# Kernel tuning notes

Measured on AMD Instinct MI355X. Metric: run time of the kernel, lower is better.

## Reference

```python
import jax, jax.numpy as jnp
import numpy as np

B, T, D, R, WP, WF, NS = 32, 256, 512, 4, 8, 8, 2
N = B * T


def _build_graph():
    # Windowed dialog graph: edge j -> i for j in [i-WP, i+WF], j != i.
    # rel = (0 if same speaker else 2) + (1 if j > i else 0)
    rng = np.random.RandomState(0)
    spk = rng.randint(0, NS, size=(B, T))
    src, dst, rel = [], [], []
    for b in range(B):
        off = b * T
        for i in range(T):
            for j in range(max(0, i - WP), min(T - 1, i + WF) + 1):
                if j == i:
                    continue
                r = (0 if spk[b, j] == spk[b, i] else 2) + int(j > i)
                src.append(off + j)
                dst.append(off + i)
                rel.append(r)
    return np.array([src, dst], dtype=np.int32), np.array(rel, dtype=np.int32)


def setup_inputs() -> dict:
    key = jax.random.key(0)
    ks = jax.random.split(key, 16)
    ei, et = _build_graph()
    s = 0.02
    f32 = jnp.float32
    return {
        "x": jax.random.normal(ks[0], (B, T, D), f32),
        "edge_index": jnp.asarray(ei),
        "edge_type": jnp.asarray(et),
        # RGCNConv params (aggr='mean', root_weight=True, bias=True)
        "W_rel": jax.random.normal(ks[1], (R, D, D), f32) * s,
        "W_root": jax.random.normal(ks[2], (D, D), f32) * s,
        "b_rgcn": jnp.zeros((D,), f32),
        # TransformerConv params (heads=1, concat=True, root_weight=True)
        "Wq": jax.random.normal(ks[3], (D, D), f32) * s,
        "bq": jnp.zeros((D,), f32),
        "Wk": jax.random.normal(ks[4], (D, D), f32) * s,
        "bk": jnp.zeros((D,), f32),
        "Wv": jax.random.normal(ks[5], (D, D), f32) * s,
        "bv": jnp.zeros((D,), f32),
        "Wskip": jax.random.normal(ks[6], (D, D), f32) * s,
        "bskip": jnp.zeros((D,), f32),
        # LayerNorm params
        "gamma": jnp.ones((D,), f32),
        "beta": jnp.zeros((D,), f32),
    }


def _gnn(x, edge_index, edge_type, W_rel, W_root, b_rgcn,
         Wq, bq, Wk, bk, Wv, bv, Wskip, bskip, gamma, beta):
    nodes = x.reshape(N, D)  # all dia_len == T, so valid nodes = all nodes
    src, dst = edge_index[0], edge_index[1]

    # --- RGCNConv: per-relation linear + mean aggregation over each relation ---
    xW = jnp.einsum("nd,rde->nre", nodes, W_rel)          # [N, R, D]
    msg = xW[src, edge_type]                                # [E, D]
    comb = dst * R + edge_type                              # group (dst, rel)
    cnt = jax.ops.segment_sum(jnp.ones(src.shape, nodes.dtype), comb,
                              num_segments=N * R).reshape(N, R)
    inv = 1.0 / jnp.maximum(cnt, 1.0)
    msg = msg * inv[dst, edge_type][:, None]
    ho = jax.ops.segment_sum(msg, dst, num_segments=N) + nodes @ W_root + b_rgcn

    # --- TransformerConv (heads=1): edge attention + scatter-softmax ---
    q = ho @ Wq + bq
    k = ho @ Wk + bk
    v = ho @ Wv + bv
    logits = jnp.sum(q[dst] * k[src], axis=-1) / jnp.sqrt(jnp.asarray(D, ho.dtype))
    mx = jax.ops.segment_max(logits, dst, num_segments=N)
    mx = jnp.where(jnp.isfinite(mx), mx, 0.0)               # nodes w/o in-edges
    ex = jnp.exp(logits - mx[dst])
    den = jax.ops.segment_sum(ex, dst, num_segments=N)
    alpha = ex / jnp.maximum(den[dst], 1e-16)
    agg = jax.ops.segment_sum(alpha[:, None] * v[src], dst, num_segments=N)
    h = agg + ho @ Wskip + bskip

    h = jax.nn.leaky_relu(h, 0.01)                          # dropout = identity (eval)
    out = x + h.reshape(B, T, D)
    mu = out.mean(-1, keepdims=True)
    var = out.var(-1, keepdims=True)
    return (out - mu) / jnp.sqrt(var + 1e-5) * gamma + beta


def reference(x, edge_index, edge_type, W_rel, W_root, b_rgcn,
              Wq, bq, Wk, bk, Wv, bv, Wskip, bskip, gamma, beta):
    out = _gnn(x, edge_index, edge_type, W_rel, W_root, b_rgcn,
               Wq, bq, Wk, bk, Wv, bv, Wskip, bskip, gamma, beta)
    return out, jnp.asarray(0.0, x.dtype)  # graph_cl_loss == 0 in eval path
```

## Files before the change

kernel.cpp:

```cpp
#include <hip/hip_runtime.h>

typedef unsigned short u16;
typedef __attribute__((ext_vector_type(8))) short s16x8;
typedef __attribute__((ext_vector_type(4))) float f32x4;

__device__ __forceinline__ float bf2f(u16 u) {
  union { unsigned int i; float f; } v; v.i = ((unsigned int)u) << 16; return v.f;
}
__device__ __forceinline__ u16 f2bf(float f) {
  union { float f; unsigned int i; } v; v.f = f;
  unsigned int r = (v.i + 0x7FFFu + ((v.i >> 16) & 1u)) >> 16;
  return (u16)r;
}
__device__ __forceinline__ void async16(const void* g, void* l) {
  __builtin_amdgcn_global_load_lds((const __attribute__((address_space(1))) void*)g,
                                   (__attribute__((address_space(3))) void*)l, 16, 0, 0);
}

__global__ __launch_bounds__(256) void prep_kernel(
    const float* __restrict__ W_rel, const float* __restrict__ W_root,
    const float* __restrict__ Wq, const float* __restrict__ Wk,
    const float* __restrict__ Wv, const float* __restrict__ Wskip,
    const float* __restrict__ bq, const float* __restrict__ bk,
    const float* __restrict__ bv, const float* __restrict__ bskip,
    const float* __restrict__ x,
    u16* __restrict__ Bt1, u16* __restrict__ Bt2, float* __restrict__ bias2,
    u16* __restrict__ Acat, int Nn,
    const int* __restrict__ dst, int E, int* __restrict__ rs, int* __restrict__ re)
{
  const int b = (int)blockIdx.x;
  const int tid = threadIdx.x;
  if (b < 576) {
    __shared__ float tile[64][65];
    const float* S;
    u16* D;
    int ldD;
    long dbase;
    if (b < 320) {
      const int kt = b >> 3, et = b & 7;
      const int r0 = kt * 64, c0 = et * 64;
      S = (r0 < 2048) ? (W_rel + (long)r0 * 512 + c0)
                      : (W_root + (long)(r0 - 2048) * 512 + c0);
      D = Bt1; ldD = 2560; dbase = (long)c0 * 2560 + r0;
    } else {
      const int b2 = b - 320;
      const int jt = b2 >> 3, kt = b2 & 7;
      const int j0 = jt * 64, k0 = kt * 64;
      const int which = j0 >> 9, col0 = j0 & 511;
      const float* W = (which == 0) ? Wq : (which == 1) ? Wk : (which == 2) ? Wv : Wskip;
      S = W + (long)k0 * 512 + col0;
      D = Bt2; ldD = 512; dbase = (long)j0 * 512 + k0;
    }
    const int lc = tid & 63;
#pragma unroll
    for (int i = 0; i < 16; ++i) {
      const int r = (tid >> 6) * 16 + i;
      tile[r][lc] = S[(long)r * 512 + lc];
    }
    __syncthreads();
    const int oc2 = (tid & 31) * 2;
#pragma unroll
    for (int i = 0; i < 8; ++i) {
      const int orow = (tid >> 5) + i * 8;
      const unsigned int pk = (unsigned int)f2bf(tile[oc2][orow]) |
                              ((unsigned int)f2bf(tile[oc2 + 1][orow]) << 16);
      *(unsigned int*)(D + dbase + (long)orow * ldD + oc2) = pk;
    }
  } else if (b == 576) {
#pragma unroll
    for (int i = 0; i < 8; ++i) {
      const int j = tid + i * 256;
      const int which = j >> 9, col = j & 511;
      const float* bb = (which == 0) ? bq : (which == 1) ? bk : (which == 2) ? bv : bskip;
      bias2[j] = bb[col];
    }
  } else if (b < 4673) {
    const long u = ((long)(b - 577) * 256 + tid) * 4;
    if (u < (long)Nn * 512) {
      const float4 v = *(const float4*)(x + u);
      const unsigned int p0 = (unsigned int)f2bf(v.x) | ((unsigned int)f2bf(v.y) << 16);
      const unsigned int p1 = (unsigned int)f2bf(v.z) | ((unsigned int)f2bf(v.w) << 16);
      unsigned int* dp = (unsigned int*)(Acat + ((long)(u >> 9)) * 2560 + 2048 + (u & 511));
      dp[0] = p0; dp[1] = p1;
    }
  } else {
    const int e = (b - 4673) * 256 + tid;
    if (e < E) {
      const int d = dst[e];
      if (e == 0 || dst[e - 1] != d) rs[d] = e;
      if (e == E - 1 || dst[e + 1] != d) re[d] = e + 1;
    }
  }
}

__global__ __launch_bounds__(256) void aggregate_kernel(
    const u16* __restrict__ Acat_ro, const int* __restrict__ src,
    const int* __restrict__ etype, const int* __restrict__ rs,
    const int* __restrict__ re, u16* __restrict__ Acat)
{
  __shared__ int s_src[16];
  __shared__ int s_rel[16];
  const int q = (int)gridDim.x >> 3;
  const int bid = (int)blockIdx.x;
  const int i = (bid & 7) * q + (bid >> 3);
  const int tid = threadIdx.x;
  const int s = rs[i];
  int nE = re[i] - s;
  if (nE > 16) nE = 16;
  if (tid < nE) { s_src[tid] = src[s + tid]; s_rel[tid] = etype[s + tid]; }
  __syncthreads();

  float2 acc[4] = {};
  int cnt[4] = {0, 0, 0, 0};
  for (int t = 0; t < nE; ++t) {
    const int sj = s_src[t];
    const int rel = s_rel[t];
    const unsigned int pk = *(const unsigned int*)(Acat_ro + (long)sj * 2560 + 2048 + tid * 2);
    const float vx = bf2f((u16)pk), vy = bf2f((u16)(pk >> 16));
#pragma unroll
    for (int r = 0; r < 4; ++r)
      if (rel == r) { acc[r].x += vx; acc[r].y += vy; cnt[r]++; }
  }

  const long base = (long)i * 2560 + tid * 2;
#pragma unroll
  for (int r = 0; r < 4; ++r) {
    const float inv = 1.0f / fmaxf((float)cnt[r], 1.0f);
    const unsigned int pk = ((unsigned int)f2bf(acc[r].y * inv) << 16) | f2bf(acc[r].x * inv);
    *(unsigned int*)(Acat + base + r * 512) = pk;
  }
}

__global__ __launch_bounds__(512, 4) void gemm_bt_kernel(
    const u16* __restrict__ A, const u16* __restrict__ Bt,
    const float* __restrict__ bias, u16* __restrict__ C,
    const int M, const int N, const int K)
{
  __shared__ u16 lds[2][2][128 * 64];
  const int tid = threadIdx.x;
  const int lane = tid & 63, wid = tid >> 6;
  const int nbn = N >> 7;
  const int q = (int)gridDim.x >> 3;
  const int bid = (int)blockIdx.x;
  const int swz = (bid & 7) * q + (bid >> 3);
  const int bm = swz / nbn, bn = swz % nbn;
  const int wr = wid >> 2, wc = wid & 3;

  f32x4 acc[4][2] = {};

  const int srow = tid >> 3;
  const int sch = tid & 7;
  const long a_row0 = (long)bm * 128;
  const long b_row0 = (long)bn * 128;
  const int lds_wbase = wid * 512;

  auto STAGE = [&](int buf, int kt) {
#pragma unroll
    for (int it = 0; it < 2; ++it) {
      const int row = it * 64 + srow;
      const int lch = sch ^ (row & 7);
      async16(A  + (a_row0 + row) * K + kt + lch * 8, &lds[buf][0][it * 4096 + lds_wbase]);
      async16(Bt + (b_row0 + row) * K + kt + lch * 8, &lds[buf][1][it * 4096 + lds_wbase]);
    }
  };

  const int nt = K >> 6;
  STAGE(0, 0);
  int cur = 0;
  for (int t = 0; t < nt; ++t) {
    asm volatile("s_waitcnt vmcnt(0)" ::: "memory");
    __builtin_amdgcn_s_barrier();
    if (t + 1 < nt) STAGE(cur ^ 1, (t + 1) << 6);
#pragma unroll
    for (int kk = 0; kk < 2; ++kk) {
      s16x8 af[4], bfr[2];
#pragma unroll
      for (int mi = 0; mi < 4; ++mi) {
        const int row = wr * 64 + mi * 16 + (lane & 15);
        const int cb = (kk * 64 + ((lane >> 4) << 4)) ^ ((row & 7) << 4);
        af[mi] = *(const s16x8*)((const char*)&lds[cur][0][0] + row * 128 + cb);
      }
#pragma unroll
      for (int ni = 0; ni < 2; ++ni) {
        const int row = wc * 32 + ni * 16 + (lane & 15);
        const int cb = (kk * 64 + ((lane >> 4) << 4)) ^ ((row & 7) << 4);
        bfr[ni] = *(const s16x8*)((const char*)&lds[cur][1][0] + row * 128 + cb);
      }
      __builtin_amdgcn_s_setprio(1);
#pragma unroll
      for (int mi = 0; mi < 4; ++mi)
#pragma unroll
        for (int ni = 0; ni < 2; ++ni)
          acc[mi][ni] = __builtin_amdgcn_mfma_f32_16x16x32_bf16(af[mi], bfr[ni], acc[mi][ni], 0, 0, 0);
      __builtin_amdgcn_s_setprio(0);
    }
    cur ^= 1;
  }

#pragma unroll
  for (int mi = 0; mi < 4; ++mi) {
    const int row0 = bm * 128 + wr * 64 + mi * 16 + ((lane >> 4) << 2);
#pragma unroll
    for (int ni = 0; ni < 2; ++ni) {
      const int col = bn * 128 + wc * 32 + ni * 16 + (lane & 15);
      const float bv = bias[col];
#pragma unroll
      for (int j = 0; j < 4; ++j)
        C[(long)(row0 + j) * N + col] = f2bf(acc[mi][ni][j] + bv);
    }
  }
}

__global__ __launch_bounds__(512, 2) void gemm256_kernel(
    const u16* __restrict__ A, const u16* __restrict__ Bt,
    const float* __restrict__ bias, u16* __restrict__ C,
    const int M, const int N, const int K)
{
  __shared__ u16 lds[2][2][256 * 64];
  const int tid = threadIdx.x;
  const int lane = tid & 63, wid = tid >> 6;
  const int nbn = N >> 8;
  const int q = (int)gridDim.x >> 3;
  const int bid = (int)blockIdx.x;
  const int swz = (bid & 7) * q + (bid >> 3);
  const int bm = swz / nbn, bn = swz % nbn;
  const int wr = wid >> 2, wc = wid & 3;

  f32x4 acc[8][4] = {};

  const int srow = tid >> 3;
  const int sch = tid & 7;
  const long a_row0 = (long)bm * 256;
  const long b_row0 = (long)bn * 256;
  const int lds_wbase = wid * 512;

  auto STAGE = [&](int buf, int kt) {
#pragma unroll
    for (int it = 0; it < 4; ++it) {
      const int row = it * 64 + srow;
      const int lch = sch ^ (srow & 7);
      async16(A  + (a_row0 + row) * K + kt + lch * 8, &lds[buf][0][it * 4096 + lds_wbase]);
      async16(Bt + (b_row0 + row) * K + kt + lch * 8, &lds[buf][1][it * 4096 + lds_wbase]);
    }
  };

  const int nt = K >> 6;
  STAGE(0, 0);
  int cur = 0;
  for (int t = 0; t < nt; ++t) {
    asm volatile("s_waitcnt vmcnt(0)" ::: "memory");
    __builtin_amdgcn_s_barrier();
    s16x8 bfr[4][2];
#pragma unroll
    for (int p = 0; p < 4; ++p) {
      s16x8 af[2][2];
#pragma unroll
      for (int i2 = 0; i2 < 2; ++i2) {
        const int row = wr * 128 + (p * 2 + i2) * 16 + (lane & 15);
#pragma unroll
        for (int kk = 0; kk < 2; ++kk) {
          const int cb = (kk * 64 + ((lane >> 4) << 4)) ^ ((row & 7) << 4);
          af[i2][kk] = *(const s16x8*)((const char*)&lds[cur][0][0] + row * 128 + cb);
        }
      }
      if (p == 0) {
#pragma unroll
        for (int ni = 0; ni < 4; ++ni) {
          const int row = wc * 64 + ni * 16 + (lane & 15);
#pragma unroll
          for (int kk = 0; kk < 2; ++kk) {
            const int cb = (kk * 64 + ((lane >> 4) << 4)) ^ ((row & 7) << 4);
            bfr[ni][kk] = *(const s16x8*)((const char*)&lds[cur][1][0] + row * 128 + cb);
          }
        }
        if (t + 1 < nt) STAGE(cur ^ 1, (t + 1) << 6);
      }
      __builtin_amdgcn_s_barrier();
      asm volatile("s_waitcnt lgkmcnt(0)" ::: "memory");
      __builtin_amdgcn_sched_barrier(0);
      __builtin_amdgcn_s_setprio(1);
#pragma unroll
      for (int i2 = 0; i2 < 2; ++i2)
#pragma unroll
        for (int ni = 0; ni < 4; ++ni)
#pragma unroll
          for (int kk = 0; kk < 2; ++kk)
            acc[p * 2 + i2][ni] = __builtin_amdgcn_mfma_f32_16x16x32_bf16(
                af[i2][kk], bfr[ni][kk], acc[p * 2 + i2][ni], 0, 0, 0);
      __builtin_amdgcn_s_setprio(0);
      __builtin_amdgcn_s_barrier();
    }
    cur ^= 1;
  }

#pragma unroll
  for (int mi = 0; mi < 8; ++mi) {
    const int row0 = bm * 256 + wr * 128 + mi * 16 + ((lane >> 4) << 2);
#pragma unroll
    for (int ni = 0; ni < 4; ++ni) {
      const int col = bn * 256 + wc * 64 + ni * 16 + (lane & 15);
      const float bv = bias[col];
#pragma unroll
      for (int j = 0; j < 4; ++j)
        C[(long)(row0 + j) * N + col] = f2bf(acc[mi][ni][j] + bv);
    }
  }
}

__global__ __launch_bounds__(256) void attn_wave_kernel(
    const u16* __restrict__ qkvs, const int* __restrict__ src,
    const int* __restrict__ rs, const int* __restrict__ re,
    const float* __restrict__ x, const float* __restrict__ gamma,
    const float* __restrict__ beta, float* __restrict__ out,
    float* __restrict__ scl)
{
  __shared__ float sm[4][16];
  __shared__ int s_src[4][16];
  const int bid = (int)blockIdx.x;
  const int tid = threadIdx.x;
  const int lane = tid & 63, wid = tid >> 6;
  const int q = (int)gridDim.x >> 3;
  const int blk = (bid & 7) * q + (bid >> 3);
  const int i = blk * 4 + wid;
  if (bid == 0 && tid == 0) scl[0] = 0.0f;

  const int s0 = rs[i];
  int ne = re[i] - s0;
  if (ne > 16) ne = 16;
  const int g16 = lane & 15;
  const int eg  = lane >> 4;
  if (lane < ne) s_src[wid][lane] = src[s0 + lane];

  float qv[32];
#pragma unroll
  for (int c = 0; c < 4; ++c) {
    const s16x8 q8 = *(const s16x8*)(qkvs + (long)i * 2048 + c * 128 + g16 * 8);
#pragma unroll
    for (int u = 0; u < 8; ++u) qv[c * 8 + u] = bf2f((u16)q8[u]);
  }

#pragma unroll
  for (int round = 0; round < 4; ++round) {
    const int e = round * 4 + eg;
    float dp = 0.f;
    if (e < ne) {
      const long rb = (long)s_src[wid][e] * 2048 + 512;
#pragma unroll
      for (int c = 0; c < 4; ++c) {
        const s16x8 k8 = *(const s16x8*)(qkvs + rb + c * 128 + g16 * 8);
#pragma unroll
        for (int u = 0; u < 8; ++u) dp += qv[c * 8 + u] * bf2f((u16)k8[u]);
      }
    }
#pragma unroll
    for (int m = 1; m <= 8; m <<= 1) dp += __shfl_xor(dp, m);
    if (g16 == 0 && e < ne) sm[wid][e] = dp * 0.04419417382415922f;
  }
  {
    const float v = (lane < ne) ? sm[wid][lane] : -1e30f;
    float mx = v;
#pragma unroll
    for (int m = 1; m <= 8; m <<= 1) mx = fmaxf(mx, __shfl_xor(mx, m, 16));
    const float ex = (lane < ne) ? expf(v - mx) : 0.f;
    float den = ex;
#pragma unroll
    for (int m = 1; m <= 8; m <<= 1) den += __shfl_xor(den, m, 16);
    if (lane < ne) sm[wid][lane] = ex / fmaxf(den, 1e-16f);
  }

  const int d8 = lane * 8;
  float a[8] = {};
  for (int e = 0; e < ne; ++e) {
    const float al = sm[wid][e];
    const s16x8 v8 = *(const s16x8*)(qkvs + (long)s_src[wid][e] * 2048 + 1024 + d8);
#pragma unroll
    for (int u = 0; u < 8; ++u) a[u] += al * bf2f((u16)v8[u]);
  }
  const s16x8 sk8 = *(const s16x8*)(qkvs + (long)i * 2048 + 1536 + d8);
  const float4 x0 = *(const float4*)(x + (long)i * 512 + d8);
  const float4 x1 = *(const float4*)(x + (long)i * 512 + d8 + 4);
  float o[8];
  float s = 0.f, s2 = 0.f;
#pragma unroll
  for (int u = 0; u < 8; ++u) {
    float h = a[u] + bf2f((u16)sk8[u]);
    h = (h > 0.f) ? h : 0.01f * h;
    const float xx = (u < 4) ? ((const float*)&x0)[u] : ((const float*)&x1)[u - 4];
    o[u] = xx + h;
    s += o[u];
    s2 += o[u] * o[u];
  }
#pragma unroll
  for (int m = 32; m >= 1; m >>= 1) { s += __shfl_xor(s, m); s2 += __shfl_xor(s2, m); }
  const float mean = s * (1.f / 512.f);
  const float var = s2 * (1.f / 512.f) - mean * mean;
  const float rstd = rsqrtf(var + 1e-5f);
  const float4 g0 = *(const float4*)(gamma + d8), g1 = *(const float4*)(gamma + d8 + 4);
  const float4 b0 = *(const float4*)(beta + d8),  b1 = *(const float4*)(beta + d8 + 4);
  float4 r0, r1;
  r0.x = (o[0] - mean) * rstd * g0.x + b0.x;
  r0.y = (o[1] - mean) * rstd * g0.y + b0.y;
  r0.z = (o[2] - mean) * rstd * g0.z + b0.z;
  r0.w = (o[3] - mean) * rstd * g0.w + b0.w;
  r1.x = (o[4] - mean) * rstd * g1.x + b1.x;
  r1.y = (o[5] - mean) * rstd * g1.y + b1.y;
  r1.z = (o[6] - mean) * rstd * g1.z + b1.z;
  r1.w = (o[7] - mean) * rstd * g1.w + b1.w;
  *(float4*)(out + (long)i * 512 + d8) = r0;
  *(float4*)(out + (long)i * 512 + d8 + 4) = r1;
}

extern "C" void kernel_launch(void* const* d_in, const int* in_sizes, int n_in,
                              void* d_out, int out_size, void* d_ws, size_t ws_size,
                              hipStream_t stream) {
  const float* x      = (const float*)d_in[0];
  const int*   ei     = (const int*)d_in[1];
  const int*   et     = (const int*)d_in[2];
  const float* W_rel  = (const float*)d_in[3];
  const float* W_root = (const float*)d_in[4];
  const float* b_rgcn = (const float*)d_in[5];
  const float* Wq     = (const float*)d_in[6];
  const float* bq     = (const float*)d_in[7];
  const float* Wk     = (const float*)d_in[8];
  const float* bk     = (const float*)d_in[9];
  const float* Wv     = (const float*)d_in[10];
  const float* bv     = (const float*)d_in[11];
  const float* Wskip  = (const float*)d_in[12];
  const float* bskip  = (const float*)d_in[13];
  const float* gamma  = (const float*)d_in[14];
  const float* beta   = (const float*)d_in[15];
  const int E  = in_sizes[2];
  const int Nn = in_sizes[0] / 512;
  const int* srcA = ei;
  const int* dstA = ei + E;

  char* p = (char*)d_ws;
  u16* Acat   = (u16*)p;   p += (size_t)Nn * 2560 * 2;
  u16* Bt1    = (u16*)p;   p += (size_t)512 * 2560 * 2;
  u16* Bt2    = (u16*)p;   p += (size_t)2048 * 512 * 2;
  float* bias2= (float*)p; p += (size_t)2048 * 4;
  u16* ho     = (u16*)p;   p += (size_t)Nn * 512 * 2;
  u16* qkvs   = (u16*)p;   p += (size_t)Nn * 2048 * 2;
  int* rs     = (int*)p;   p += (size_t)Nn * 4;
  int* re     = (int*)p;   p += (size_t)Nn * 4;

  const int FB = (E + 255) / 256;
  const int prep_blocks = 4673 + FB;

  prep_kernel<<<prep_blocks, 256, 0, stream>>>(W_rel, W_root, Wq, Wk, Wv, Wskip,
                                               bq, bk, bv, bskip, x, Bt1, Bt2, bias2, Acat, Nn,
                                               dstA, E, rs, re);
  aggregate_kernel<<<Nn, 256, 0, stream>>>(Acat, srcA, et, rs, re, Acat);
  gemm_bt_kernel<<<(Nn / 128) * (512 >> 7), 512, 0, stream>>>(Acat, Bt1, b_rgcn, ho, Nn, 512, 2560);
  gemm256_kernel<<<(Nn / 256) * (2048 >> 8), 512, 0, stream>>>(ho, Bt2, bias2, qkvs, Nn, 2048, 512);
  attn_wave_kernel<<<Nn / 4, 256, 0, stream>>>(qkvs, srcA, rs, re, x, gamma, beta,
                                               (float*)d_out, (float*)d_out + (size_t)Nn * 512);
}
```

Baseline: 114.8 us.

## Double K-tile depth in GEMM and restructure LDS read/MFMA phases with barriers

```diff
diff --git a/kernel.cpp b/kernel.cpp
--- a/kernel.cpp
+++ b/kernel.cpp
@@ -131,12 +131,12 @@
   }
 }
 
-__global__ __launch_bounds__(512, 4) void gemm_bt_kernel(
+__global__ __launch_bounds__(512, 2) void gemm_bt_kernel(
     const u16* __restrict__ A, const u16* __restrict__ Bt,
     const float* __restrict__ bias, u16* __restrict__ C,
     const int M, const int N, const int K)
 {
-  __shared__ u16 lds[2][2][128 * 64];
+  __shared__ u16 lds[2][2][128 * 128];
   const int tid = threadIdx.x;
   const int lane = tid & 63, wid = tid >> 6;
   const int nbn = N >> 7;
@@ -148,51 +148,66 @@
 
   f32x4 acc[4][2] = {};
 
-  const int srow = tid >> 3;
-  const int sch = tid & 7;
   const long a_row0 = (long)bm * 128;
   const long b_row0 = (long)bn * 128;
-  const int lds_wbase = wid * 512;
 
   auto STAGE = [&](int buf, int kt) {
 #pragma unroll
-    for (int it = 0; it < 2; ++it) {
-      const int row = it * 64 + srow;
-      const int lch = sch ^ (row & 7);
-      async16(A  + (a_row0 + row) * K + kt + lch * 8, &lds[buf][0][it * 4096 + lds_wbase]);
-      async16(Bt + (b_row0 + row) * K + kt + lch * 8, &lds[buf][1][it * 4096 + lds_wbase]);
+    for (int it = 0; it < 4; ++it) {
+      const int rbase = it * 32 + wid * 4;
+      const int row = rbase + (lane >> 4);
+      const int lch = (lane & 15) ^ (row & 7);
+      async16(A  + (a_row0 + row) * K + kt + lch * 8, &lds[buf][0][rbase * 128]);
+      async16(Bt + (b_row0 + row) * K + kt + lch * 8, &lds[buf][1][rbase * 128]);
     }
   };
 
-  const int nt = K >> 6;
+  const int nt = K >> 7;
   STAGE(0, 0);
   int cur = 0;
   for (int t = 0; t < nt; ++t) {
     asm volatile("s_waitcnt vmcnt(0)" ::: "memory");
     __builtin_amdgcn_s_barrier();
-    if (t + 1 < nt) STAGE(cur ^ 1, (t + 1) << 6);
-#pragma unroll
-    for (int kk = 0; kk < 2; ++kk) {
-      s16x8 af[4], bfr[2];
+    s16x8 bfr[2][4];
+#pragma unroll
+    for (int p = 0; p < 2; ++p) {
+      s16x8 af[4][2];
 #pragma unroll
       for (int mi = 0; mi < 4; ++mi) {
         const int row = wr * 64 + mi * 16 + (lane & 15);
-        const int cb = (kk * 64 + ((lane >> 4) << 4)) ^ ((row & 7) << 4);
-        af[mi] = *(const s16x8*)((const char*)&lds[cur][0][0] + row * 128 + cb);
+#pragma unroll
+        for (int k2 = 0; k2 < 2; ++k2) {
+          const int kk = p * 2 + k2;
+          const int cb = (kk * 64 + ((lane >> 4) << 4)) ^ ((row & 7) << 4);
+          af[mi][k2] = *(const s16x8*)((const char*)&lds[cur][0][0] + row * 256 + cb);
+        }
       }
-#pragma unroll
-      for (int ni = 0; ni < 2; ++ni) {
-        const int row = wc * 32 + ni * 16 + (lane & 15);
-        const int cb = (kk * 64 + ((lane >> 4) << 4)) ^ ((row & 7) << 4);
-        bfr[ni] = *(const s16x8*)((const char*)&lds[cur][1][0] + row * 128 + cb);
+      if (p == 0) {
+#pragma unroll
+        for (int ni = 0; ni < 2; ++ni) {
+          const int row = wc * 32 + ni * 16 + (lane & 15);
+#pragma unroll
+          for (int kk = 0; kk < 4; ++kk) {
+            const int cb = (kk * 64 + ((lane >> 4) << 4)) ^ ((row & 7) << 4);
+            bfr[ni][kk] = *(const s16x8*)((const char*)&lds[cur][1][0] + row * 256 + cb);
+          }
+        }
+        if (t + 1 < nt) STAGE(cur ^ 1, (t + 1) << 7);
       }
+      __builtin_amdgcn_s_barrier();
+      asm volatile("s_waitcnt lgkmcnt(0)" ::: "memory");
+      __builtin_amdgcn_sched_barrier(0);
       __builtin_amdgcn_s_setprio(1);
 #pragma unroll
-      for (int mi = 0; mi < 4; ++mi)
-#pragma unroll
-        for (int ni = 0; ni < 2; ++ni)
-          acc[mi][ni] = __builtin_amdgcn_mfma_f32_16x16x32_bf16(af[mi], bfr[ni], acc[mi][ni], 0, 0, 0);
+      for (int k2 = 0; k2 < 2; ++k2)
+#pragma unroll
+        for (int mi = 0; mi < 4; ++mi)
+#pragma unroll
+          for (int ni = 0; ni < 2; ++ni)
+            acc[mi][ni] = __builtin_amdgcn_mfma_f32_16x16x32_bf16(
+                af[mi][k2], bfr[ni][p * 2 + k2], acc[mi][ni], 0, 0, 0);
       __builtin_amdgcn_s_setprio(0);
+      __builtin_amdgcn_s_barrier();
     }
     cur ^= 1;
   }
```

Result: slower. 117.9 us (+2.7%).

## Split-K the RGCN GEMM into two halves with a separate bf16 reduce kernel

Applied to the files above, without the earlier changes.

```diff
diff --git a/kernel.cpp b/kernel.cpp
--- a/kernel.cpp
+++ b/kernel.cpp
@@ -131,49 +131,50 @@
   }
 }
 
-__global__ __launch_bounds__(512, 4) void gemm_bt_kernel(
+__global__ __launch_bounds__(256, 2) void gemm_splitk_kernel(
     const u16* __restrict__ A, const u16* __restrict__ Bt,
-    const float* __restrict__ bias, u16* __restrict__ C,
-    const int M, const int N, const int K)
+    u16* __restrict__ Cp0, const int M, const int N, const int K)
 {
   __shared__ u16 lds[2][2][128 * 64];
   const int tid = threadIdx.x;
   const int lane = tid & 63, wid = tid >> 6;
-  const int nbn = N >> 7;
   const int q = (int)gridDim.x >> 3;
   const int bid = (int)blockIdx.x;
   const int swz = (bid & 7) * q + (bid >> 3);
-  const int bm = swz / nbn, bn = swz % nbn;
-  const int wr = wid >> 2, wc = wid & 3;
-
-  f32x4 acc[4][2] = {};
-
-  const int srow = tid >> 3;
-  const int sch = tid & 7;
+  const int bm = swz >> 3;
+  const int v = swz & 7;
+  const int bn = v >> 1, kh = v & 1;
+  const int wr = wid >> 1, wc = wid & 1;
+
+  f32x4 acc[4][4] = {};
+
   const long a_row0 = (long)bm * 128;
   const long b_row0 = (long)bn * 128;
-  const int lds_wbase = wid * 512;
+  const int k0 = kh * (K >> 1);
+  const int lrow8 = lane >> 3;
+  const int lch   = lane & 7;
 
   auto STAGE = [&](int buf, int kt) {
 #pragma unroll
-    for (int it = 0; it < 2; ++it) {
-      const int row = it * 64 + srow;
-      const int lch = sch ^ (row & 7);
-      async16(A  + (a_row0 + row) * K + kt + lch * 8, &lds[buf][0][it * 4096 + lds_wbase]);
-      async16(Bt + (b_row0 + row) * K + kt + lch * 8, &lds[buf][1][it * 4096 + lds_wbase]);
+    for (int it = 0; it < 4; ++it) {
+      const int row0 = wid * 32 + it * 8;
+      const int row  = row0 + lrow8;
+      const int sch  = lch ^ (row & 7);
+      async16(A  + (a_row0 + row) * K + kt + sch * 8, &lds[buf][0][row0 * 64]);
+      async16(Bt + (b_row0 + row) * K + kt + sch * 8, &lds[buf][1][row0 * 64]);
     }
   };
 
-  const int nt = K >> 6;
-  STAGE(0, 0);
+  const int nt = (K >> 1) >> 6;
+  STAGE(0, k0);
   int cur = 0;
   for (int t = 0; t < nt; ++t) {
     asm volatile("s_waitcnt vmcnt(0)" ::: "memory");
     __builtin_amdgcn_s_barrier();
-    if (t + 1 < nt) STAGE(cur ^ 1, (t + 1) << 6);
+    if (t + 1 < nt) STAGE(cur ^ 1, k0 + ((t + 1) << 6));
 #pragma unroll
     for (int kk = 0; kk < 2; ++kk) {
-      s16x8 af[4], bfr[2];
+      s16x8 af[4], bfr[4];
 #pragma unroll
       for (int mi = 0; mi < 4; ++mi) {
         const int row = wr * 64 + mi * 16 + (lane & 15);
@@ -181,8 +182,8 @@
         af[mi] = *(const s16x8*)((const char*)&lds[cur][0][0] + row * 128 + cb);
       }
 #pragma unroll
-      for (int ni = 0; ni < 2; ++ni) {
-        const int row = wc * 32 + ni * 16 + (lane & 15);
+      for (int ni = 0; ni < 4; ++ni) {
+        const int row = wc * 64 + ni * 16 + (lane & 15);
         const int cb = (kk * 64 + ((lane >> 4) << 4)) ^ ((row & 7) << 4);
         bfr[ni] = *(const s16x8*)((const char*)&lds[cur][1][0] + row * 128 + cb);
       }
@@ -190,25 +191,40 @@
 #pragma unroll
       for (int mi = 0; mi < 4; ++mi)
 #pragma unroll
-        for (int ni = 0; ni < 2; ++ni)
+        for (int ni = 0; ni < 4; ++ni)
           acc[mi][ni] = __builtin_amdgcn_mfma_f32_16x16x32_bf16(af[mi], bfr[ni], acc[mi][ni], 0, 0, 0);
       __builtin_amdgcn_s_setprio(0);
     }
     cur ^= 1;
   }
 
+  u16* Cp = Cp0 + (long)kh * M * N;
 #pragma unroll
   for (int mi = 0; mi < 4; ++mi) {
     const int row0 = bm * 128 + wr * 64 + mi * 16 + ((lane >> 4) << 2);
 #pragma unroll
-    for (int ni = 0; ni < 2; ++ni) {
-      const int col = bn * 128 + wc * 32 + ni * 16 + (lane & 15);
-      const float bv = bias[col];
+    for (int ni = 0; ni < 4; ++ni) {
+      const int col = bn * 128 + wc * 64 + ni * 16 + (lane & 15);
 #pragma unroll
       for (int j = 0; j < 4; ++j)
-        C[(long)(row0 + j) * N + col] = f2bf(acc[mi][ni][j] + bv);
-    }
-  }
+        Cp[(long)(row0 + j) * N + col] = f2bf(acc[mi][ni][j]);
+    }
+  }
+}
+
+__global__ __launch_bounds__(256) void reduce_ho_kernel(
+    const u16* __restrict__ h0, const u16* __restrict__ h1,
+    const float* __restrict__ bias, u16* __restrict__ ho)
+{
+  const long e8 = ((long)blockIdx.x * 256 + threadIdx.x) * 8;
+  const int col = (int)(e8 & 511);
+  const s16x8 a = *(const s16x8*)(h0 + e8);
+  const s16x8 b = *(const s16x8*)(h1 + e8);
+  s16x8 r;
+#pragma unroll
+  for (int u = 0; u < 8; ++u)
+    r[u] = (short)f2bf(bf2f((u16)a[u]) + bf2f((u16)b[u]) + bias[col + u]);
+  *(s16x8*)(ho + e8) = r;
 }
 
 __global__ __launch_bounds__(512, 2) void gemm256_kernel(
@@ -443,6 +459,7 @@
   u16* qkvs   = (u16*)p;   p += (size_t)Nn * 2048 * 2;
   int* rs     = (int*)p;   p += (size_t)Nn * 4;
   int* re     = (int*)p;   p += (size_t)Nn * 4;
+  u16* hop    = (u16*)p;   p += (size_t)2 * Nn * 512 * 2;
 
   const int FB = (E + 255) / 256;
   const int prep_blocks = 4673 + FB;
@@ -451,7 +468,8 @@
                                                bq, bk, bv, bskip, x, Bt1, Bt2, bias2, Acat, Nn,
                                                dstA, E, rs, re);
   aggregate_kernel<<<Nn, 256, 0, stream>>>(Acat, srcA, et, rs, re, Acat);
-  gemm_bt_kernel<<<(Nn / 128) * (512 >> 7), 512, 0, stream>>>(Acat, Bt1, b_rgcn, ho, Nn, 512, 2560);
+  gemm_splitk_kernel<<<(Nn / 128) * 4 * 2, 256, 0, stream>>>(Acat, Bt1, hop, Nn, 512, 2560);
+  reduce_ho_kernel<<<Nn * 512 / 2048, 256, 0, stream>>>(hop, hop + (size_t)Nn * 512, b_rgcn, ho);
   gemm256_kernel<<<(Nn / 256) * (2048 >> 8), 512, 0, stream>>>(ho, Bt2, bias2, qkvs, Nn, 2048, 512);
   attn_wave_kernel<<<Nn / 4, 256, 0, stream>>>(qkvs, srcA, rs, re, x, gamma, beta,
                                                (float*)d_out, (float*)d_out + (size_t)Nn * 512);
```

Result: slower. 119.3 us (+3.9%).
